# Kernel optimization log

Measured on AMD Instinct MI355X. Metric: run time of the kernel, lower is better.

## Reference

```python
import jax, jax.numpy as jnp
import numpy as np

S, B, D, H = 2048, 2, 1024, 16
DK = D // H
E, F = 8, 4096


def layernorm(x, g, b, eps=1e-5):
    mu = x.mean(-1, keepdims=True)
    var = x.var(-1, keepdims=True)
    return (x - mu) / jnp.sqrt(var + eps) * g + b


def setup_inputs() -> dict:
    key = jax.random.key(0)
    ks = jax.random.split(key, 10)
    s = 0.02
    rn = lambda k, shape: jax.random.normal(k, shape, jnp.float32) * s
    return dict(
        x=jax.random.normal(ks[0], (S, B, D), jnp.float32),
        ln1_g=jnp.ones((D,), jnp.float32), ln1_b=jnp.zeros((D,), jnp.float32),
        ln2_g=jnp.ones((D,), jnp.float32), ln2_b=jnp.zeros((D,), jnp.float32),
        wq=rn(ks[1], (D, D)), bq=jnp.zeros((D,), jnp.float32),
        wk=rn(ks[2], (D, D)), bk=jnp.zeros((D,), jnp.float32),
        wv=rn(ks[3], (D, D)), bv=jnp.zeros((D,), jnp.float32),
        wo=rn(ks[4], (D, D)), bo=jnp.zeros((D,), jnp.float32),
        w_gate=rn(ks[5], (D, E)), b_gate=jnp.zeros((E,), jnp.float32),
        w1=rn(ks[6], (E, D, F)), b1=jnp.zeros((E, F), jnp.float32),
        w2=rn(ks[7], (E, F, D)), b2=jnp.zeros((E, D), jnp.float32),
        mask=jnp.ones((S, S, B), jnp.bool_),
    )


def reference(x, ln1_g, ln1_b, ln2_g, ln2_b, wq, bq, wk, bk, wv, bv, wo, bo,
              w_gate, b_gate, w1, b1, w2, b2, mask):
    scale = 1.0 / np.sqrt(DK).astype(np.float32)
    # --- self attention (pre-norm) ---
    z = layernorm(x, ln1_g, ln1_b)
    q = (z @ wq + bq).reshape(S, B, H, DK)
    k = (z @ wk + bk).reshape(S, B, H, DK)
    v = (z @ wv + bv).reshape(S, B, H, DK)
    scores = jnp.einsum('sbhd,tbhd->stbh', q, k) * scale  # [Sq,Sk,B,H]
    scores = jnp.where(mask[:, :, :, None], scores, -jnp.inf)
    attn = jax.nn.softmax(scores, axis=1)  # softmax over key axis (dim=1)
    o = jnp.einsum('stbh,tbhd->sbhd', attn, v).reshape(S, B, D)
    x = x + (o @ wo + bo)
    # --- switch (top-1) MoE FFN (pre-norm) ---
    z = layernorm(x, ln2_g, ln2_b)
    flat = z.reshape(-1, D)  # [T, D], T = S*B
    probs = jax.nn.softmax(flat @ w_gate + b_gate, axis=-1)  # [T, E]
    pmax = probs.max(-1)
    routes = probs.argmax(-1)
    onehot = jax.nn.one_hot(routes, E, dtype=flat.dtype)  # [T, E]
    # dense dispatch: compute every expert, combine with one-hot mask
    h = jax.nn.relu(jnp.einsum('td,edf->etf', flat, w1) + b1[:, None, :])
    y = jnp.einsum('etf,efd->etd', h, w2) + b2[:, None, :]
    ff = jnp.einsum('etd,te->td', y, onehot) * pmax[:, None]
    out = x + ff.reshape(S, B, D)
    counts = onehot.sum(0)  # tokens per expert
    route_prob_sum = probs.sum(0)
    n_dropped = jnp.array(0, jnp.int32)  # drop_tokens=False
    return out, counts, route_prob_sum, n_dropped, pmax
```

## Files before the change

### kernel.cpp

```cpp
#include <hip/hip_runtime.h>

#define S_LEN 2048
#define B_SZ 2
#define D_DIM 1024
#define H_HEADS 16
#define DK_DIM 64
#define E_EXP 8
#define F_DIM 4096
#define T_TOK 4096

typedef unsigned short ush;
typedef __bf16 bf16x8 __attribute__((ext_vector_type(8)));
typedef float f32x4 __attribute__((ext_vector_type(4)));

__device__ __forceinline__ ush f2bf(float f) {
  union { __bf16 h; ush u; } cv;
  cv.h = (__bf16)f;
  return cv.u;
}

__device__ __forceinline__ float bf2f(ush u) {
  union { unsigned int i; float f; } cv;
  cv.i = ((unsigned int)u) << 16;
  return cv.f;
}

__device__ __forceinline__ void split2(float v, ush& h, ush& l) {
  ush hh = f2bf(v);
  h = hh;
  l = f2bf(v - bf2f(hh));
}

__device__ __forceinline__ void gload16(const void* g, void* l) {
  __builtin_amdgcn_global_load_lds(
      (const __attribute__((address_space(1))) unsigned int*)g,
      (__attribute__((address_space(3))) unsigned int*)l, 16, 0, 0);
}

#define MFMA(a, b, c) __builtin_amdgcn_mfma_f32_16x16x32_bf16(a, b, c, 0, 0, 0)

template <int CTRL>
__device__ __forceinline__ float dpp_mov(float x) {
  return __builtin_bit_cast(float,
      __builtin_amdgcn_update_dpp(0, __builtin_bit_cast(int, x), CTRL, 0xF, 0xF,
                                  true));
}
__device__ __forceinline__ float rmax16(float x) {
  x = fmaxf(x, dpp_mov<0xB1>(x));
  x = fmaxf(x, dpp_mov<0x4E>(x));
  x = fmaxf(x, dpp_mov<0x141>(x));
  x = fmaxf(x, dpp_mov<0x140>(x));
  return x;
}
__device__ __forceinline__ float rsum16(float x) {
  x += dpp_mov<0xB1>(x);
  x += dpp_mov<0x4E>(x);
  x += dpp_mov<0x141>(x);
  x += dpp_mov<0x140>(x);
  return x;
}

__global__ __launch_bounds__(256) void ln1_split(const float* __restrict__ x,
    const float* __restrict__ g, const float* __restrict__ b,
    ush* __restrict__ zh, ush* __restrict__ zl) {
  int t = blockIdx.x;
  float4 v = ((const float4*)(x + (size_t)t * D_DIM))[threadIdx.x];
  float s = v.x + v.y + v.z + v.w;
  float s2 = v.x * v.x + v.y * v.y + v.z * v.z + v.w * v.w;
#pragma unroll
  for (int off = 32; off > 0; off >>= 1) {
    s += __shfl_down(s, off);
    s2 += __shfl_down(s2, off);
  }
  __shared__ float red[8];
  int wid = threadIdx.x >> 6;
  if ((threadIdx.x & 63) == 0) { red[wid] = s; red[4 + wid] = s2; }
  __syncthreads();
  float sum = red[0] + red[1] + red[2] + red[3];
  float sq = red[4] + red[5] + red[6] + red[7];
  float mu = sum * (1.0f / D_DIM);
  float var = sq * (1.0f / D_DIM) - mu * mu;
  float rstd = rsqrtf(var + 1e-5f);
  float4 gg = ((const float4*)g)[threadIdx.x];
  float4 bb = ((const float4*)b)[threadIdx.x];
  float o[4];
  o[0] = (v.x - mu) * rstd * gg.x + bb.x;
  o[1] = (v.y - mu) * rstd * gg.y + bb.y;
  o[2] = (v.z - mu) * rstd * gg.z + bb.z;
  o[3] = (v.w - mu) * rstd * gg.w + bb.w;
  ushort4 uh, ul;
  split2(o[0], uh.x, ul.x); split2(o[1], uh.y, ul.y);
  split2(o[2], uh.z, ul.z); split2(o[3], uh.w, ul.w);
  *(ushort4*)(zh + (size_t)t * D_DIM + threadIdx.x * 4) = uh;
  *(ushort4*)(zl + (size_t)t * D_DIM + threadIdx.x * 4) = ul;
}

__global__ __launch_bounds__(256) void transpose_split(const float* __restrict__ in,
    ush* __restrict__ outh, ush* __restrict__ outl, int R, int C) {
  __shared__ float tile[32][33];
  int c0 = blockIdx.x * 32, r0 = blockIdx.y * 32;
  int tx = threadIdx.x & 31, ty = threadIdx.x >> 5;
#pragma unroll
  for (int i = 0; i < 4; i++)
    tile[ty + i * 8][tx] = in[(size_t)(r0 + ty + i * 8) * C + c0 + tx];
  __syncthreads();
#pragma unroll
  for (int i = 0; i < 4; i++) {
    float v = tile[tx][ty + i * 8];
    ush h, l;
    split2(v, h, l);
    size_t idx = (size_t)(c0 + ty + i * 8) * R + r0 + tx;
    outh[idx] = h;
    outl[idx] = l;
  }
}

__global__ __launch_bounds__(256) void transpose_bf16(const float* __restrict__ in,
    ush* __restrict__ out, int R, int C) {
  __shared__ float tile[32][33];
  int e = blockIdx.z;
  const float* ip = in + (size_t)e * R * C;
  ush* op = out + (size_t)e * R * C;
  int c0 = blockIdx.x * 32, r0 = blockIdx.y * 32;
  int tx = threadIdx.x & 31, ty = threadIdx.x >> 5;
#pragma unroll
  for (int i = 0; i < 4; i++)
    tile[ty + i * 8][tx] = ip[(size_t)(r0 + ty + i * 8) * C + c0 + tx];
  __syncthreads();
#pragma unroll
  for (int i = 0; i < 4; i++)
    op[(size_t)(c0 + ty + i * 8) * R + r0 + tx] = f2bf(tile[tx][ty + i * 8]);
}

__device__ __forceinline__ void split_gemm(const ush* __restrict__ Ah,
    const ush* __restrict__ Al, int lda, const ush* __restrict__ Bh,
    const ush* __restrict__ Bl, int ldb, int K, int tid, f32x4 acc[4][4],
    ush (*Ash)[64], ush (*Asl)[64], ush (*Bsh)[64], ush (*Bsl)[64]) {
  int lane = tid & 63, w = tid >> 6, quad = lane >> 4, ln15 = lane & 15;
  int srow = tid >> 3, pcol = (tid & 7) * 8;
  int scol = ((tid & 7) ^ (srow & 7)) * 8;
  int sw = ln15 & 7;
  int mb = (w >> 1) * 64, nb = (w & 1) * 64;
  for (int kb = 0; kb < K; kb += 64) {
    __syncthreads();
#pragma unroll
    for (int r = 0; r < 4; r++) {
      int rr = r * 32 + srow;
      gload16(Ah + (size_t)rr * lda + kb + scol, &Ash[rr][pcol]);
      gload16(Al + (size_t)rr * lda + kb + scol, &Asl[rr][pcol]);
      gload16(Bh + (size_t)rr * ldb + kb + scol, &Bsh[rr][pcol]);
      gload16(Bl + (size_t)rr * ldb + kb + scol, &Bsl[rr][pcol]);
    }
    __syncthreads();
#pragma unroll
    for (int kc = 0; kc < 2; kc++) {
      int kof = ((kc * 4 + quad) ^ sw) * 8;
      bf16x8 avh[4], avl[4], bvh[4], bvl[4];
#pragma unroll
      for (int i = 0; i < 4; i++) {
        avh[i] = *(const bf16x8*)&Ash[mb + i * 16 + ln15][kof];
        avl[i] = *(const bf16x8*)&Asl[mb + i * 16 + ln15][kof];
        bvh[i] = *(const bf16x8*)&Bsh[nb + i * 16 + ln15][kof];
        bvl[i] = *(const bf16x8*)&Bsl[nb + i * 16 + ln15][kof];
      }
#pragma unroll
      for (int mi = 0; mi < 4; mi++)
#pragma unroll
        for (int ni = 0; ni < 4; ni++) {
          acc[mi][ni] = MFMA(avh[mi], bvh[ni], acc[mi][ni]);
          acc[mi][ni] = MFMA(avh[mi], bvl[ni], acc[mi][ni]);
          acc[mi][ni] = MFMA(avl[mi], bvh[ni], acc[mi][ni]);
        }
    }
  }
}

__global__ __launch_bounds__(256) void qkv_mfma(const ush* __restrict__ zh,
    const ush* __restrict__ zl, const ush* __restrict__ wT,
    const float* __restrict__ bq, const float* __restrict__ bk,
    const float* __restrict__ bv, ush* __restrict__ qh_, ush* __restrict__ kh_,
    ush* __restrict__ vth_) {
  __shared__ ush Ash[128][64], Asl[128][64], Bsh[128][64], Bsl[128][64];
  int z = blockIdx.z;
  int m0 = blockIdx.x * 128, n0 = blockIdx.y * 128;
  const ush* Bh = wT + (size_t)z * 2097152;
  const ush* Bl = Bh + 1048576;
  const float* bias = (z == 0) ? bq : (z == 1) ? bk : bv;
  ush* outh = (z == 0) ? qh_ : (z == 1) ? kh_ : vth_;
  int tid = threadIdx.x, lane = tid & 63, w = tid >> 6;
  int quad = lane >> 4, ln15 = lane & 15;
  int mb = (w >> 1) * 64, nb = (w & 1) * 64;
  f32x4 acc[4][4] = {};
  split_gemm(zh + (size_t)m0 * D_DIM, zl + (size_t)m0 * D_DIM, D_DIM,
             Bh + (size_t)n0 * D_DIM, Bl + (size_t)n0 * D_DIM, D_DIM, D_DIM,
             tid, acc, Ash, Asl, Bsh, Bsl);
#pragma unroll
  for (int mi = 0; mi < 4; mi++)
#pragma unroll
    for (int reg = 0; reg < 4; reg++) {
      int m = m0 + mb + mi * 16 + quad * 4 + reg;
      int s = m >> 1, b = m & 1;
#pragma unroll
      for (int ni = 0; ni < 4; ni++) {
        int n = n0 + nb + ni * 16 + ln15;
        float val = acc[mi][ni][reg] + bias[n];
        ush hh, ll;
        split2(val, hh, ll);
        int h = n >> 6, dk = n & 63;
        size_t idx;
        if (z < 2) idx = ((size_t)(b * H_HEADS + h) * S_LEN + s) * DK_DIM + dk;
        else       idx = ((size_t)(b * H_HEADS + h) * DK_DIM + dk) * S_LEN + s;
        outh[idx] = hh;
        outh[idx + 4194304] = ll;
      }
    }
}

__global__ __launch_bounds__(256, 2) void attn_mfma(const ush* __restrict__ qh,
    const ush* __restrict__ ql, const ush* __restrict__ kh,
    const ush* __restrict__ kl, const ush* __restrict__ vth,
    const ush* __restrict__ vtl, ush* __restrict__ oh, ush* __restrict__ ol) {
  int bh = blockIdx.y, q0 = blockIdx.x * 128;
  const size_t hoff = (size_t)bh * S_LEN * DK_DIM;
  __shared__ float4 smemv[3072];
  ush* Ph_ = (ush*)smemv;
  ush* Kh_ = (ush*)smemv + 8192;
  ush* Kl_ = (ush*)smemv + 12288;
  ush* Vh_ = (ush*)smemv + 16384;
  ush* Vl_ = (ush*)smemv + 20480;
  int tid = threadIdx.x, lane = tid & 63, w = tid >> 6;
  int quad = lane >> 4, ln15 = lane & 15;
  int srow = tid >> 3;
  int schunk = tid & 7;
  int gch = (schunk ^ (srow & 7)) * 8;
  int sw = ln15 & 7;
#pragma unroll
  for (int p = 0; p < 2; p++) {
    int r = p * 32 + srow;
    gload16(kh + hoff + (size_t)r * DK_DIM + gch, Kh_ + r * 64 + schunk * 8);
    gload16(kl + hoff + (size_t)r * DK_DIM + gch, Kl_ + r * 64 + schunk * 8);
  }
  bf16x8 Qf[2][2][2];
#pragma unroll
  for (int mi = 0; mi < 2; mi++)
#pragma unroll
    for (int kc = 0; kc < 2; kc++) {
      size_t qidx = hoff + (size_t)(q0 + w * 32 + mi * 16 + ln15) * DK_DIM +
                    (kc * 4 + quad) * 8;
      Qf[mi][kc][0] = *(const bf16x8*)(qh + qidx);
      Qf[mi][kc][1] = *(const bf16x8*)(ql + qidx);
    }
  f32x4 Oacc[2][4] = {};
  float m_i[2][4], l_i[2][4];
#pragma unroll
  for (int mi = 0; mi < 2; mi++)
#pragma unroll
    for (int r = 0; r < 4; r++) { m_i[mi][r] = -3e38f; l_i[mi][r] = 0.f; }
  const float cs = 0.18033688f;
  __syncthreads();
  for (int kt = 0; kt < S_LEN / 64; kt++) {
#pragma unroll
    for (int p = 0; p < 2; p++) {
      int r = p * 32 + srow;
      gload16(vth + hoff + (size_t)r * S_LEN + kt * 64 + gch,
              Vh_ + r * 64 + schunk * 8);
      gload16(vtl + hoff + (size_t)r * S_LEN + kt * 64 + gch,
              Vl_ + r * 64 + schunk * 8);
    }
    f32x4 S[2][4] = {};
#pragma unroll
    for (int kc = 0; kc < 2; kc++) {
      int ch = ((kc * 4 + quad) ^ sw) * 8;
      bf16x8 bkh[4], bkl[4];
#pragma unroll
      for (int ni = 0; ni < 4; ni++) {
        int row = ni * 16 + ln15;
        bkh[ni] = *(const bf16x8*)(Kh_ + row * 64 + ch);
        bkl[ni] = *(const bf16x8*)(Kl_ + row * 64 + ch);
      }
      __builtin_amdgcn_s_setprio(1);
#pragma unroll
      for (int mi = 0; mi < 2; mi++)
#pragma unroll
        for (int ni = 0; ni < 4; ni++) {
          S[mi][ni] = MFMA(Qf[mi][kc][0], bkh[ni], S[mi][ni]);
          S[mi][ni] = MFMA(Qf[mi][kc][0], bkl[ni], S[mi][ni]);
          S[mi][ni] = MFMA(Qf[mi][kc][1], bkh[ni], S[mi][ni]);
        }
      __builtin_amdgcn_s_setprio(0);
    }
    float mt[2][4];
#pragma unroll
    for (int mi = 0; mi < 2; mi++)
#pragma unroll
      for (int reg = 0; reg < 4; reg++) {
        float m = fmaxf(fmaxf(S[mi][0][reg], S[mi][1][reg]),
                        fmaxf(S[mi][2][reg], S[mi][3][reg]));
        mt[mi][reg] = rmax16(m);
      }
    float growth = -3e38f;
#pragma unroll
    for (int mi = 0; mi < 2; mi++)
#pragma unroll
      for (int reg = 0; reg < 4; reg++)
        growth = fmaxf(growth, mt[mi][reg] - m_i[mi][reg]);
    if (__any(growth > 44.3614195f)) {
#pragma unroll
      for (int mi = 0; mi < 2; mi++)
#pragma unroll
        for (int reg = 0; reg < 4; reg++) {
          float mnew = fmaxf(m_i[mi][reg], mt[mi][reg]);
          float a = __builtin_amdgcn_exp2f(cs * (m_i[mi][reg] - mnew));
          m_i[mi][reg] = mnew;
          l_i[mi][reg] *= a;
#pragma unroll
          for (int ni = 0; ni < 4; ni++) Oacc[mi][ni][reg] *= a;
        }
    }
    float ncm[2][4], ls[2][4] = {};
#pragma unroll
    for (int mi = 0; mi < 2; mi++)
#pragma unroll
      for (int reg = 0; reg < 4; reg++) ncm[mi][reg] = cs * m_i[mi][reg];
#pragma unroll
    for (int mi = 0; mi < 2; mi++)
#pragma unroll
      for (int ni = 0; ni < 4; ni++)
#pragma unroll
        for (int reg = 0; reg < 4; reg++) {
          float p = __builtin_amdgcn_exp2f(
              fmaf(S[mi][ni][reg], cs, -ncm[mi][reg]));
          ush hh = f2bf(p);
          ls[mi][reg] += bf2f(hh);
          int row = w * 32 + mi * 16 + quad * 4 + reg;
          int cph = ((ni * 2 + (ln15 >> 3)) ^ ((quad * 4 + reg) & 7)) * 8 + (ln15 & 7);
          Ph_[row * 64 + cph] = hh;
        }
#pragma unroll
    for (int mi = 0; mi < 2; mi++)
#pragma unroll
      for (int reg = 0; reg < 4; reg++)
        l_i[mi][reg] += rsum16(ls[mi][reg]);
    __syncthreads();
    if (kt + 1 < S_LEN / 64) {
#pragma unroll
      for (int p = 0; p < 2; p++) {
        int r = p * 32 + srow;
        gload16(kh + hoff + (size_t)((kt + 1) * 64 + r) * DK_DIM + gch,
                Kh_ + r * 64 + schunk * 8);
        gload16(kl + hoff + (size_t)((kt + 1) * 64 + r) * DK_DIM + gch,
                Kl_ + r * 64 + schunk * 8);
      }
    }
#pragma unroll
    for (int kc = 0; kc < 2; kc++) {
      int ch = ((kc * 4 + quad) ^ sw) * 8;
      bf16x8 ap[2], bvh[4], bvl[4];
#pragma unroll
      for (int mi = 0; mi < 2; mi++) {
        int row = w * 32 + mi * 16 + ln15;
        ap[mi] = *(const bf16x8*)(Ph_ + row * 64 + ch);
      }
#pragma unroll
      for (int ni = 0; ni < 4; ni++) {
        int row = ni * 16 + ln15;
        bvh[ni] = *(const bf16x8*)(Vh_ + row * 64 + ch);
        bvl[ni] = *(const bf16x8*)(Vl_ + row * 64 + ch);
      }
      __builtin_amdgcn_s_setprio(1);
#pragma unroll
      for (int mi = 0; mi < 2; mi++)
#pragma unroll
        for (int ni = 0; ni < 4; ni++) {
          Oacc[mi][ni] = MFMA(ap[mi], bvh[ni], Oacc[mi][ni]);
          Oacc[mi][ni] = MFMA(ap[mi], bvl[ni], Oacc[mi][ni]);
        }
      __builtin_amdgcn_s_setprio(0);
    }
    __syncthreads();
  }
  float inv[2][4];
#pragma unroll
  for (int mi = 0; mi < 2; mi++)
#pragma unroll
    for (int reg = 0; reg < 4; reg++) inv[mi][reg] = 1.0f / l_i[mi][reg];
  int b = bh >> 4, h = bh & 15;
#pragma unroll
  for (int mi = 0; mi < 2; mi++)
#pragma unroll
    for (int ni = 0; ni < 4; ni++)
#pragma unroll
      for (int reg = 0; reg < 4; reg++) {
        float ov = Oacc[mi][ni][reg] * inv[mi][reg];
        int s = q0 + w * 32 + mi * 16 + quad * 4 + reg;
        int col = h * DK_DIM + ni * 16 + ln15;
        size_t idx = (size_t)(s * B_SZ + b) * D_DIM + col;
        ush hh, ll;
        split2(ov, hh, ll);
        oh[idx] = hh;
        ol[idx] = ll;
      }
}

__global__ __launch_bounds__(256) void wo_mfma(const ush* __restrict__ oh,
    const ush* __restrict__ ol, const ush* __restrict__ woTh,
    const float* __restrict__ bo, const float* __restrict__ x,
    float* __restrict__ out) {
  __shared__ ush Ash[128][64], Asl[128][64], Bsh[128][64], Bsl[128][64];
  int m0 = blockIdx.x * 128, n0 = blockIdx.y * 128;
  const ush* Bl = woTh + 1048576;
  int tid = threadIdx.x, lane = tid & 63, w = tid >> 6;
  int quad = lane >> 4, ln15 = lane & 15;
  int mb = (w >> 1) * 64, nb = (w & 1) * 64;
  f32x4 acc[4][4] = {};
  split_gemm(oh + (size_t)m0 * D_DIM, ol + (size_t)m0 * D_DIM, D_DIM,
             woTh + (size_t)n0 * D_DIM, Bl + (size_t)n0 * D_DIM, D_DIM, D_DIM,
             tid, acc, Ash, Asl, Bsh, Bsl);
#pragma unroll
  for (int mi = 0; mi < 4; mi++)
#pragma unroll
    for (int reg = 0; reg < 4; reg++) {
      int m = m0 + mb + mi * 16 + quad * 4 + reg;
#pragma unroll
      for (int ni = 0; ni < 4; ni++) {
        int n = n0 + nb + ni * 16 + ln15;
        size_t idx = (size_t)m * D_DIM + n;
        out[idx] = x[idx] + acc[mi][ni][reg] + bo[n];
      }
    }
}

__global__ __launch_bounds__(256) void moe1_mfma(const ush* __restrict__ zb,
    const ush* __restrict__ w1t, const float* __restrict__ b1,
    const int* __restrict__ list, const int* __restrict__ offs,
    ush* __restrict__ h) {
  int e = blockIdx.x;
  int n0 = blockIdx.y * 128;
  int mhalf = blockIdx.z;
  int off = offs[e], cnt = offs[e + 1] - off;
  __shared__ ush As[2][128][64], Bs[2][128][64];
  int tid = threadIdx.x, lane = tid & 63, w = tid >> 6;
  int srw = w * 8 + (lane >> 3);
  int colb = (lane & 7) * 8;
  int scol = ((lane & 7) ^ (srw & 7)) * 8;
  int mb = (w >> 1) * 64, nb = (w & 1) * 64;
  int quad = lane >> 4, ln15 = lane & 15, sw = ln15 & 7;
  const ush* gB[4];
#pragma unroll
  for (int r = 0; r < 4; r++)
    gB[r] = w1t + ((size_t)e * F_DIM + n0 + r * 32 + srw) * D_DIM + scol;
  const float* be = b1 + (size_t)e * F_DIM;
  for (int m0 = mhalf * 128; m0 < cnt; m0 += 256) {
    const ush* gA[4];
#pragma unroll
    for (int r = 0; r < 4; r++) {
      int ra = m0 + r * 32 + srw; if (ra > cnt - 1) ra = cnt - 1;
      gA[r] = zb + (size_t)list[off + ra] * D_DIM + scol;
    }
#define STG1(buf, kb) do { _Pragma("unroll")                                   \
    for (int r = 0; r < 4; r++) {                                              \
      gload16(gA[r] + (kb), &As[buf][r * 32 + srw][colb]);                     \
      gload16(gB[r] + (kb), &Bs[buf][r * 32 + srw][colb]); } } while (0)
    STG1(0, 0);
    __syncthreads();
    f32x4 acc[4][4] = {};
    for (int ki = 0; ki < 16; ki++) {
      int cur = ki & 1;
      if (ki < 15) STG1(cur ^ 1, (ki + 1) * 64);
#pragma unroll
      for (int kc = 0; kc < 2; kc++) {
        int kof = ((kc * 4 + quad) ^ sw) * 8;
        bf16x8 av[4], bv[4];
#pragma unroll
        for (int i = 0; i < 4; i++) {
          av[i] = *(const bf16x8*)&As[cur][mb + i * 16 + ln15][kof];
          bv[i] = *(const bf16x8*)&Bs[cur][nb + i * 16 + ln15][kof];
        }
#pragma unroll
        for (int mi = 0; mi < 4; mi++)
#pragma unroll
          for (int ni = 0; ni < 4; ni++)
            acc[mi][ni] = MFMA(av[mi], bv[ni], acc[mi][ni]);
      }
      __syncthreads();
    }
#undef STG1
#pragma unroll
    for (int mi = 0; mi < 4; mi++)
#pragma unroll
      for (int reg = 0; reg < 4; reg++) {
        int lm = m0 + mb + mi * 16 + quad * 4 + reg;
        if (lm < cnt) {
#pragma unroll
          for (int ni = 0; ni < 4; ni++) {
            int n = n0 + nb + ni * 16 + ln15;
            float v = acc[mi][ni][reg] + be[n];
            h[(size_t)(off + lm) * F_DIM + n] = f2bf(fmaxf(v, 0.f));
          }
        }
      }
  }
}

__global__ __launch_bounds__(256) void moe2_mfma(const ush* __restrict__ hb,
    const ush* __restrict__ w2t, const float* __restrict__ b2,
    const int* __restrict__ list, const int* __restrict__ offs,
    const float* __restrict__ pmax, float* __restrict__ out) {
  int e = blockIdx.x;
  int n0 = blockIdx.y * 128;
  int ks = blockIdx.z >> 1;
  int mhalf = blockIdx.z & 1;
  int off = offs[e], cnt = offs[e + 1] - off;
  size_t kbase = (size_t)ks * 1024;
  __shared__ ush As[2][128][64], Bs[2][128][64];
  int tid = threadIdx.x, lane = tid & 63, w = tid >> 6;
  int srw = w * 8 + (lane >> 3);
  int colb = (lane & 7) * 8;
  int scol = ((lane & 7) ^ (srw & 7)) * 8;
  int mb = (w >> 1) * 64, nb = (w & 1) * 64;
  int quad = lane >> 4, ln15 = lane & 15, sw = ln15 & 7;
  const ush* gB[4];
#pragma unroll
  for (int r = 0; r < 4; r++)
    gB[r] = w2t + ((size_t)e * D_DIM + n0 + r * 32 + srw) * F_DIM + kbase + scol;
  const float* be = b2 + (size_t)e * D_DIM;
  for (int m0 = mhalf * 128; m0 < cnt; m0 += 256) {
    const ush* gA[4];
#pragma unroll
    for (int r = 0; r < 4; r++) {
      int ra = m0 + r * 32 + srw; if (ra > cnt - 1) ra = cnt - 1;
      gA[r] = hb + (size_t)(off + ra) * F_DIM + kbase + scol;
    }
#define STG2(buf, kb) do { _Pragma("unroll")                                   \
    for (int r = 0; r < 4; r++) {                                              \
      gload16(gA[r] + (kb), &As[buf][r * 32 + srw][colb]);                     \
      gload16(gB[r] + (kb), &Bs[buf][r * 32 + srw][colb]); } } while (0)
    STG2(0, 0);
    __syncthreads();
    f32x4 acc[4][4] = {};
    for (int ki = 0; ki < 16; ki++) {
      int cur = ki & 1;
      if (ki < 15) STG2(cur ^ 1, (ki + 1) * 64);
#pragma unroll
      for (int kc = 0; kc < 2; kc++) {
        int kof = ((kc * 4 + quad) ^ sw) * 8;
        bf16x8 av[4], bv[4];
#pragma unroll
        for (int i = 0; i < 4; i++) {
          av[i] = *(const bf16x8*)&As[cur][mb + i * 16 + ln15][kof];
          bv[i] = *(const bf16x8*)&Bs[cur][nb + i * 16 + ln15][kof];
        }
#pragma unroll
        for (int mi = 0; mi < 4; mi++)
#pragma unroll
          for (int ni = 0; ni < 4; ni++)
            acc[mi][ni] = MFMA(av[mi], bv[ni], acc[mi][ni]);
      }
      __syncthreads();
    }
#undef STG2
#pragma unroll
    for (int mi = 0; mi < 4; mi++)
#pragma unroll
      for (int reg = 0; reg < 4; reg++) {
        int lm = m0 + mb + mi * 16 + quad * 4 + reg;
        if (lm < cnt) {
          int tok = list[off + lm];
          float p = pmax[tok];
#pragma unroll
          for (int ni = 0; ni < 4; ni++) {
            int n = n0 + nb + ni * 16 + ln15;
            float v = acc[mi][ni][reg];
            if (ks == 0) v += be[n];
            atomicAdd(&out[(size_t)tok * D_DIM + n], v * p);
          }
        }
      }
  }
}

__global__ __launch_bounds__(256) void ln2_gate(const float* __restrict__ x,
    const float* __restrict__ g, const float* __restrict__ b,
    const float* __restrict__ wg, const float* __restrict__ bg,
    ush* __restrict__ zb, float* __restrict__ pmax_out, int* __restrict__ route,
    float* __restrict__ rps_partial) {
  int t = blockIdx.x;
  float4 v = ((const float4*)(x + (size_t)t * D_DIM))[threadIdx.x];
  float s = v.x + v.y + v.z + v.w;
  float s2 = v.x * v.x + v.y * v.y + v.z * v.z + v.w * v.w;
#pragma unroll
  for (int off = 32; off > 0; off >>= 1) {
    s += __shfl_down(s, off);
    s2 += __shfl_down(s2, off);
  }
  __shared__ float red[8];
  int wid = threadIdx.x >> 6;
  if ((threadIdx.x & 63) == 0) { red[wid] = s; red[4 + wid] = s2; }
  __syncthreads();
  float sum = red[0] + red[1] + red[2] + red[3];
  float sq = red[4] + red[5] + red[6] + red[7];
  float mu = sum * (1.0f / D_DIM);
  float var = sq * (1.0f / D_DIM) - mu * mu;
  float rstd = rsqrtf(var + 1e-5f);
  float4 gg = ((const float4*)g)[threadIdx.x];
  float4 bb = ((const float4*)b)[threadIdx.x];
  float zz[4];
  zz[0] = (v.x - mu) * rstd * gg.x + bb.x;
  zz[1] = (v.y - mu) * rstd * gg.y + bb.y;
  zz[2] = (v.z - mu) * rstd * gg.z + bb.z;
  zz[3] = (v.w - mu) * rstd * gg.w + bb.w;
  ushort4 u;
  u.x = f2bf(zz[0]); u.y = f2bf(zz[1]); u.z = f2bf(zz[2]); u.w = f2bf(zz[3]);
  *(ushort4*)(zb + (size_t)t * D_DIM + threadIdx.x * 4) = u;
  int d0 = threadIdx.x * 4;
  float acc[8] = {};
  const float* w0 = wg + (size_t)d0 * E_EXP;
#pragma unroll
  for (int i = 0; i < 4; i++)
#pragma unroll
    for (int e = 0; e < 8; e++)
      acc[e] += zz[i] * w0[i * 8 + e];
#pragma unroll
  for (int off = 32; off > 0; off >>= 1)
#pragma unroll
    for (int e = 0; e < 8; e++) acc[e] += __shfl_down(acc[e], off);
  __shared__ float red2[4][8];
  if ((threadIdx.x & 63) == 0)
#pragma unroll
    for (int e = 0; e < 8; e++) red2[threadIdx.x >> 6][e] = acc[e];
  __syncthreads();
  if (threadIdx.x == 0) {
    float lg[8];
#pragma unroll
    for (int e = 0; e < 8; e++)
      lg[e] = red2[0][e] + red2[1][e] + red2[2][e] + red2[3][e] + bg[e];
    float mx = lg[0];
    int am = 0;
#pragma unroll
    for (int e = 1; e < 8; e++)
      if (lg[e] > mx) { mx = lg[e]; am = e; }
    float se = 0.f, pe[8];
#pragma unroll
    for (int e = 0; e < 8; e++) { pe[e] = expf(lg[e] - mx); se += pe[e]; }
    float inv = 1.0f / se;
    pmax_out[t] = inv;
    route[t] = am;
#pragma unroll
    for (int e = 0; e < 8; e++) rps_partial[(size_t)t * 8 + e] = pe[e] * inv;
  }
}

__global__ __launch_bounds__(256) void reduce_gate(const float* __restrict__ rps_partial,
    const int* __restrict__ route, float* __restrict__ rps, int* __restrict__ counts) {
  int e = blockIdx.x;
  float s = 0.f;
  int c = 0;
  for (int t = threadIdx.x; t < T_TOK; t += 256) {
    s += rps_partial[(size_t)t * 8 + e];
    c += (route[t] == e) ? 1 : 0;
  }
#pragma unroll
  for (int off = 32; off > 0; off >>= 1) {
    s += __shfl_down(s, off);
    c += __shfl_down(c, off);
  }
  __shared__ float sred[4];
  __shared__ int cred[4];
  int wid = threadIdx.x >> 6;
  if ((threadIdx.x & 63) == 0) { sred[wid] = s; cred[wid] = c; }
  __syncthreads();
  if (threadIdx.x == 0) {
    rps[e] = sred[0] + sred[1] + sred[2] + sred[3];
    counts[e] = cred[0] + cred[1] + cred[2] + cred[3];
  }
}

__global__ void init_kernel(int* cursor) {
  int i = threadIdx.x;
  if (i < E_EXP) cursor[i] = 0;
}

__global__ void offsets_kernel(const int* counts, int* offs, float* counts_f, float* ndrop) {
  if (threadIdx.x == 0) {
    int o = 0;
    for (int e = 0; e < E_EXP; e++) { offs[e] = o; o += counts[e]; }
    offs[E_EXP] = o;
    for (int e = 0; e < E_EXP; e++) counts_f[e] = (float)counts[e];
    *ndrop = 0.f;
  }
}

__global__ void scatter_kernel(const int* __restrict__ route, const int* __restrict__ offs,
                               int* __restrict__ cursor, int* __restrict__ list) {
  int t = blockIdx.x * 256 + threadIdx.x;
  int lane = threadIdx.x & 63;
  int e = (t < T_TOK) ? route[t] : -1;
#pragma unroll
  for (int ex = 0; ex < E_EXP; ex++) {
    unsigned long long mask = __ballot(e == ex);
    int cntw = __popcll(mask);
    if (cntw) {
      int leader = __ffsll((unsigned long long)mask) - 1;
      int base = 0;
      if (lane == leader) base = atomicAdd(&cursor[ex], cntw);
      base = __shfl(base, leader);
      if (e == ex) {
        int rank = __popcll(mask & ((1ull << lane) - 1));
        list[offs[ex] + base + rank] = t;
      }
    }
  }
}

extern "C" void kernel_launch(void* const* d_in, const int* in_sizes, int n_in,
                              void* d_out, int out_size, void* d_ws, size_t ws_size,
                              hipStream_t stream) {
  const float* x = (const float*)d_in[0];
  const float* ln1_g = (const float*)d_in[1];
  const float* ln1_b = (const float*)d_in[2];
  const float* ln2_g = (const float*)d_in[3];
  const float* ln2_b = (const float*)d_in[4];
  const float* wq = (const float*)d_in[5];
  const float* bq = (const float*)d_in[6];
  const float* wk = (const float*)d_in[7];
  const float* bk = (const float*)d_in[8];
  const float* wv = (const float*)d_in[9];
  const float* bv = (const float*)d_in[10];
  const float* wo = (const float*)d_in[11];
  const float* bo = (const float*)d_in[12];
  const float* wg = (const float*)d_in[13];
  const float* bg = (const float*)d_in[14];
  const float* w1 = (const float*)d_in[15];
  const float* b1 = (const float*)d_in[16];
  const float* w2 = (const float*)d_in[17];
  const float* b2 = (const float*)d_in[18];

  float* out = (float*)d_out;
  float* counts_f = out + (size_t)T_TOK * D_DIM;
  float* rps = counts_f + E_EXP;
  float* ndrop = rps + E_EXP;
  float* pmax = ndrop + 1;

  const size_t MB1 = 1048576;
  char* base = (char*)d_ws;
  ush* zh  = (ush*)(base + 0 * MB1);
  ush* zl  = (ush*)(base + 8 * MB1);
  ush* qh  = (ush*)(base + 16 * MB1);
  ush* ql  = (ush*)(base + 24 * MB1);
  ush* kh  = (ush*)(base + 32 * MB1);
  ush* kl  = (ush*)(base + 40 * MB1);
  ush* vth = (ush*)(base + 48 * MB1);
  ush* vtl = (ush*)(base + 56 * MB1);
  ush* wT  = (ush*)(base + 64 * MB1);
  ush* oh  = (ush*)(base + 80 * MB1);
  ush* ol  = (ush*)(base + 88 * MB1);
  ush* zb  = (ush*)(base + 64 * MB1);
  ush* hb  = (ush*)(base + 72 * MB1);
  int* route  = (int*)(base + 104 * MB1);
  int* list   = route + T_TOK;
  int* counts = list + T_TOK;
  int* offs   = counts + E_EXP;
  int* cursor = offs + E_EXP + 1;
  float* rps_partial = (float*)(base + 106 * MB1);
  ush* w1t = (ush*)(base + 0 * MB1);
  ush* w2t = (ush*)(base + 112 * MB1);

  ln1_split<<<T_TOK, 256, 0, stream>>>(x, ln1_g, ln1_b, zh, zl);
  dim3 gt(32, 32);
  transpose_split<<<gt, 256, 0, stream>>>(wq, wT + 0 * 2097152, wT + 0 * 2097152 + 1048576, D_DIM, D_DIM);
  transpose_split<<<gt, 256, 0, stream>>>(wk, wT + 1 * 2097152, wT + 1 * 2097152 + 1048576, D_DIM, D_DIM);
  transpose_split<<<gt, 256, 0, stream>>>(wv, wT + 2 * 2097152, wT + 2 * 2097152 + 1048576, D_DIM, D_DIM);
  transpose_split<<<gt, 256, 0, stream>>>(wo, wT + 3 * 2097152, wT + 3 * 2097152 + 1048576, D_DIM, D_DIM);
  dim3 gq(32, 8, 3);
  qkv_mfma<<<gq, 256, 0, stream>>>(zh, zl, wT, bq, bk, bv, qh, kh, vth);
  dim3 ga(S_LEN / 128, B_SZ * H_HEADS);
  attn_mfma<<<ga, 256, 0, stream>>>(qh, ql, kh, kl, vth, vtl, oh, ol);
  dim3 gt1(F_DIM / 32, D_DIM / 32, E_EXP);
  transpose_bf16<<<gt1, 256, 0, stream>>>(w1, w1t, D_DIM, F_DIM);
  dim3 gt2(D_DIM / 32, F_DIM / 32, E_EXP);
  transpose_bf16<<<gt2, 256, 0, stream>>>(w2, w2t, F_DIM, D_DIM);
  dim3 gw(32, 8);
  wo_mfma<<<gw, 256, 0, stream>>>(oh, ol, wT + 3 * 2097152, bo, x, out);
  init_kernel<<<1, 64, 0, stream>>>(cursor);
  ln2_gate<<<T_TOK, 256, 0, stream>>>(out, ln2_g, ln2_b, wg, bg, zb, pmax, route, rps_partial);
  reduce_gate<<<E_EXP, 256, 0, stream>>>(rps_partial, route, rps, counts);
  offsets_kernel<<<1, 64, 0, stream>>>(counts, offs, counts_f, ndrop);
  scatter_kernel<<<16, 256, 0, stream>>>(route, offs, cursor, list);
  dim3 gm1(E_EXP, F_DIM / 128, 2);
  moe1_mfma<<<gm1, 256, 0, stream>>>(zb, w1t, b1, list, offs, hb);
  dim3 gm2(E_EXP, D_DIM / 128, 8);
  moe2_mfma<<<gm2, 256, 0, stream>>>(hb, w2t, b2, list, offs, pmax, out);
}
```

Baseline: 886.4 us.

## Use vmcnt-gated barriers, MFMA priority and a flat grid in MoE GEMMs

In both MoE expert GEMM kernels, __syncthreads is replaced by an explicit s_waitcnt vmcnt(8) plus a raw s_barrier. Each wave therefore waits only for the previous stage's direct-to-LDS loads while the next stage's loads stay in flight. The MFMA block is wrapped in s_setprio(1)/s_setprio(0) so matrix work gets issue priority over waves doing loads. The 3D grids are flattened to 1D with expert index fastest, changing block scheduling order, at the risk of relying on exact load counts for correctness.

```diff
diff --git a/kernel.cpp b/kernel.cpp
--- a/kernel.cpp
+++ b/kernel.cpp
@@ -434,9 +434,10 @@
     const ush* __restrict__ w1t, const float* __restrict__ b1,
     const int* __restrict__ list, const int* __restrict__ offs,
     ush* __restrict__ h) {
-  int e = blockIdx.x;
-  int n0 = blockIdx.y * 128;
-  int mhalf = blockIdx.z;
+  int id = blockIdx.x;
+  int e = id & 7;
+  int mhalf = (id >> 3) & 1;
+  int n0 = ((id >> 4) & 31) * 128;
   int off = offs[e], cnt = offs[e + 1] - off;
   __shared__ ush As[2][128][64], Bs[2][128][64];
   int tid = threadIdx.x, lane = tid & 63, w = tid >> 6;
@@ -462,11 +463,16 @@
       gload16(gA[r] + (kb), &As[buf][r * 32 + srw][colb]);                     \
       gload16(gB[r] + (kb), &Bs[buf][r * 32 + srw][colb]); } } while (0)
     STG1(0, 0);
-    __syncthreads();
     f32x4 acc[4][4] = {};
     for (int ki = 0; ki < 16; ki++) {
       int cur = ki & 1;
-      if (ki < 15) STG1(cur ^ 1, (ki + 1) * 64);
+      if (ki < 15) {
+        STG1(cur ^ 1, (ki + 1) * 64);
+        asm volatile("s_waitcnt vmcnt(8)" ::: "memory");
+      } else {
+        asm volatile("s_waitcnt vmcnt(0)" ::: "memory");
+      }
+      __builtin_amdgcn_s_barrier();
 #pragma unroll
       for (int kc = 0; kc < 2; kc++) {
         int kof = ((kc * 4 + quad) ^ sw) * 8;
@@ -476,13 +482,15 @@
           av[i] = *(const bf16x8*)&As[cur][mb + i * 16 + ln15][kof];
           bv[i] = *(const bf16x8*)&Bs[cur][nb + i * 16 + ln15][kof];
         }
+        __builtin_amdgcn_s_setprio(1);
 #pragma unroll
         for (int mi = 0; mi < 4; mi++)
 #pragma unroll
           for (int ni = 0; ni < 4; ni++)
             acc[mi][ni] = MFMA(av[mi], bv[ni], acc[mi][ni]);
-      }
-      __syncthreads();
+        __builtin_amdgcn_s_setprio(0);
+      }
+      __builtin_amdgcn_s_barrier();
     }
 #undef STG1
 #pragma unroll
@@ -506,10 +514,11 @@
     const ush* __restrict__ w2t, const float* __restrict__ b2,
     const int* __restrict__ list, const int* __restrict__ offs,
     const float* __restrict__ pmax, float* __restrict__ out) {
-  int e = blockIdx.x;
-  int n0 = blockIdx.y * 128;
-  int ks = blockIdx.z >> 1;
-  int mhalf = blockIdx.z & 1;
+  int id = blockIdx.x;
+  int e = id & 7;
+  int mhalf = (id >> 3) & 1;
+  int n0 = ((id >> 4) & 7) * 128;
+  int ks = (id >> 7) & 3;
   int off = offs[e], cnt = offs[e + 1] - off;
   size_t kbase = (size_t)ks * 1024;
   __shared__ ush As[2][128][64], Bs[2][128][64];
@@ -536,11 +545,16 @@
       gload16(gA[r] + (kb), &As[buf][r * 32 + srw][colb]);                     \
       gload16(gB[r] + (kb), &Bs[buf][r * 32 + srw][colb]); } } while (0)
     STG2(0, 0);
-    __syncthreads();
     f32x4 acc[4][4] = {};
     for (int ki = 0; ki < 16; ki++) {
       int cur = ki & 1;
-      if (ki < 15) STG2(cur ^ 1, (ki + 1) * 64);
+      if (ki < 15) {
+        STG2(cur ^ 1, (ki + 1) * 64);
+        asm volatile("s_waitcnt vmcnt(8)" ::: "memory");
+      } else {
+        asm volatile("s_waitcnt vmcnt(0)" ::: "memory");
+      }
+      __builtin_amdgcn_s_barrier();
 #pragma unroll
       for (int kc = 0; kc < 2; kc++) {
         int kof = ((kc * 4 + quad) ^ sw) * 8;
@@ -550,13 +564,15 @@
           av[i] = *(const bf16x8*)&As[cur][mb + i * 16 + ln15][kof];
           bv[i] = *(const bf16x8*)&Bs[cur][nb + i * 16 + ln15][kof];
         }
+        __builtin_amdgcn_s_setprio(1);
 #pragma unroll
         for (int mi = 0; mi < 4; mi++)
 #pragma unroll
           for (int ni = 0; ni < 4; ni++)
             acc[mi][ni] = MFMA(av[mi], bv[ni], acc[mi][ni]);
-      }
-      __syncthreads();
+        __builtin_amdgcn_s_setprio(0);
+      }
+      __builtin_amdgcn_s_barrier();
     }
 #undef STG2
 #pragma unroll
@@ -786,8 +802,6 @@
   reduce_gate<<<E_EXP, 256, 0, stream>>>(rps_partial, route, rps, counts);
   offsets_kernel<<<1, 64, 0, stream>>>(counts, offs, counts_f, ndrop);
   scatter_kernel<<<16, 256, 0, stream>>>(route, offs, cursor, list);
-  dim3 gm1(E_EXP, F_DIM / 128, 2);
-  moe1_mfma<<<gm1, 256, 0, stream>>>(zb, w1t, b1, list, offs, hb);
-  dim3 gm2(E_EXP, D_DIM / 128, 8);
-  moe2_mfma<<<gm2, 256, 0, stream>>>(hb, w2t, b2, list, offs, pmax, out);
-}
+  moe1_mfma<<<512, 256, 0, stream>>>(zb, w1t, b1, list, offs, hb);
+  moe2_mfma<<<512, 256, 0, stream>>>(hb, w2t, b2, list, offs, pmax, out);
+}
```

New measurement: 848.5 us. 4.3% less time.
